# Kernel tuning notes

Measured on AMD Instinct MI355X. Metric: run time of the kernel, lower is better.

## Reference

```python
import jax, jax.numpy as jnp
import numpy as np

NUM_HEADS = 16
HEAD_DIM = 64  # embedding_dim 1024 / 16


def setup_inputs() -> dict:
    key = jax.random.key(0)
    k1, k2, k3, k4 = jax.random.split(key, 4)
    B, S, D = 2, 2048, 1024
    return {
        "query": jax.random.normal(k1, (B, S, D), dtype=jnp.float32),
        "key": jax.random.normal(k2, (B, S, D), dtype=jnp.float32),
        "value": jax.random.normal(k3, (B, S, D), dtype=jnp.float32),
        "W_out": jax.random.normal(k4, (D, D), dtype=jnp.float32) * (1.0 / np.sqrt(D)),
        "b_out": jnp.zeros((D,), dtype=jnp.float32),
    }


def reference(query, key, value, W_out, b_out):
    B, S, D = query.shape
    H, hd = NUM_HEADS, HEAD_DIM
    # NOTE: original forward never applies q_fc/k_fc/v_fc (transform ignores fc)
    q = query.reshape(B, S, H, hd).transpose(0, 2, 1, 3)  # [B,H,S,hd]
    k = key.reshape(B, S, H, hd).transpose(0, 2, 1, 3)
    v = value.reshape(B, S, H, hd).transpose(0, 2, 1, 3)
    scores = jnp.einsum("bhqd,bhkd->bhqk", q, k) / jnp.sqrt(jnp.float32(hd))
    probs = jax.nn.softmax(scores, axis=-1)  # mask=None, dropout=None
    ctx = jnp.einsum("bhqk,bhkd->bhqd", probs, v)
    ctx = ctx.transpose(0, 2, 1, 3).reshape(B, S, D)
    return ctx @ W_out.T + b_out
```

## Files before the change

### kernel.cpp

```cpp
#include <hip/hip_runtime.h>
#include <hip/hip_bf16.h>
#include <stdint.h>

#define NB 2
#define SEQ 2048
#define DIM 1024
#define NH 16
#define HD 64

typedef __attribute__((ext_vector_type(4))) float f32x4;
typedef __attribute__((ext_vector_type(16))) float f32x16;
typedef __attribute__((ext_vector_type(8))) short s16x8;
typedef __attribute__((ext_vector_type(4))) short s16x4;
typedef __attribute__((ext_vector_type(8))) __bf16 bf16x8;

static __device__ __forceinline__ short f2bf_rne(float x) {
  uint32_t u = __float_as_uint(x);
  u += 0x7fffu + ((u >> 16) & 1u);
  return (short)(u >> 16);
}
static __device__ __forceinline__ uint32_t pk_bf16(float a, float b) {
  __hip_bfloat162 h = __float22bfloat162_rn(float2{a, b});
  uint32_t u;
  __builtin_memcpy(&u, &h, 4);
  return u;
}
static __device__ __forceinline__ bf16x8 ldfrag(const short* p) {
  bf16x8 r;
  __builtin_memcpy(&r, p, 16);
  return r;
}
static __device__ __forceinline__ void glds16(const short* g, short* l) {
  __builtin_amdgcn_global_load_lds(
      (const __attribute__((address_space(1))) uint32_t*)g,
      (__attribute__((address_space(3))) uint32_t*)l, 16, 0, 0);
}

__global__ __launch_bounds__(256) void prep_all(const float* __restrict__ K,
                                                const float* __restrict__ V,
                                                const float* __restrict__ W,
                                                short* __restrict__ Kh,
                                                short* __restrict__ Vt,
                                                short* __restrict__ Wh) {
  __shared__ float vtile[64][65];
  const int tid = threadIdx.x;
  const int id = blockIdx.x;

  if (id >= 1024) {
    size_t idx = ((size_t)(id - 1024) * 256 + tid) * 8;
    f32x4 a = *(const f32x4*)(W + idx);
    f32x4 b = *(const f32x4*)(W + idx + 4);
    s16x8 o;
#pragma unroll
    for (int j = 0; j < 4; ++j) {
      o[j] = f2bf_rne(a[j]);
      o[4 + j] = f2bf_rne(b[j]);
    }
    *(s16x8*)(Wh + idx) = o;
    return;
  }

  const int t0 = (id & 31) * 64;
  const int bh = id >> 5;
  const int b = bh >> 4, h = bh & 15;

#pragma unroll
  for (int i = 0; i < 4; ++i) {
    int f = tid + 256 * i;
    int row = f >> 4;
    int col = (f & 15) * 4;
    const float* src = K + ((size_t)(b * SEQ + t0 + row)) * DIM + h * HD + col;
    f32x4 v = *(const f32x4*)src;
    s16x4 hi;
#pragma unroll
    for (int j = 0; j < 4; ++j) hi[j] = f2bf_rne(v[j]);
    *(s16x4*)(Kh + ((size_t)bh * SEQ + t0 + row) * HD + col) = hi;
  }
#pragma unroll
  for (int i = 0; i < 4; ++i) {
    int f = tid + 256 * i;
    int row = f >> 4;
    int col = (f & 15) * 4;
    const float* src = V + ((size_t)(b * SEQ + t0 + row)) * DIM + h * HD + col;
    f32x4 v = *(const f32x4*)src;
#pragma unroll
    for (int j = 0; j < 4; ++j) vtile[row][col + j] = v[j];
  }
  __syncthreads();
#pragma unroll
  for (int i = 0; i < 4; ++i) {
    int idx = tid + 256 * i;
    int d = idx >> 4;
    int kb = (idx & 15) * 4;
    int kp = (kb & ~12) | ((kb & 4) << 1) | ((kb & 8) >> 1);
    s16x4 o4;
#pragma unroll
    for (int j = 0; j < 4; ++j) o4[j] = f2bf_rne(vtile[kb + j][d]);
    *(s16x4*)(Vt + ((size_t)bh * HD + d) * SEQ + t0 + kp) = o4;
  }
}

#define QSCALE (0.125f * 1.44269504088896340736f)
#define NT_KV 32

static __device__ __forceinline__ f32x16 qk32(const short* kb, int kvh, int l32,
                                              int hl, const bf16x8* qh) {
  f32x16 s;
#pragma unroll
  for (int r = 0; r < 16; ++r) s[r] = 0.f;
#pragma unroll
  for (int ks = 0; ks < 4; ++ks) {
    bf16x8 kf =
        ldfrag(kb + (kvh * 32 + l32) * 64 + (((ks * 2 + hl) ^ (l32 & 7)) * 8));
    s = __builtin_amdgcn_mfma_f32_32x32x16_bf16(kf, qh[ks], s, 0, 0, 0);
  }
  return s;
}

static __device__ __forceinline__ void exppv32(const f32x16& sf, const short* vb,
                                               int kvh, int l32, int hl,
                                               f32x16* acc, float& den0,
                                               float& den1) {
#pragma unroll
  for (int tp = 0; tp < 2; ++tp) {
    uint32_t w[4];
#pragma unroll
    for (int j2 = 0; j2 < 4; ++j2) {
      float p0 = __builtin_amdgcn_exp2f(sf[tp * 8 + j2 * 2]);
      float p1 = __builtin_amdgcn_exp2f(sf[tp * 8 + j2 * 2 + 1]);
      den0 += p0;
      den1 += p1;
      w[j2] = pk_bf16(p0, p1);
    }
    bf16x8 pa;
    __builtin_memcpy(&pa, w, 16);
    const int ksg = kvh * 2 + tp;
#pragma unroll
    for (int dt = 0; dt < 2; ++dt) {
      bf16x8 vf = ldfrag(vb + (dt * 32 + l32) * 64 +
                         (((ksg * 2 + hl) ^ (l32 & 7)) * 8));
      acc[dt] =
          __builtin_amdgcn_mfma_f32_32x32x16_bf16(pa, vf, acc[dt], 0, 0, 0);
    }
  }
}

__global__ __launch_bounds__(512, 4) void attn(const float* __restrict__ Q,
                                               const short* __restrict__ Kh,
                                               const short* __restrict__ Vt,
                                               short* __restrict__ Ch) {
  __shared__ __align__(16) short kbuf[2][4096];
  __shared__ __align__(16) short vbuf[2][4096];
  __shared__ float dsh[8][64];

  const int tid = threadIdx.x;
  const int wv = tid >> 6, ln = tid & 63;
  const int l32 = ln & 31, hl = ln >> 5;
  const int qsub = wv >> 1, kvh = wv & 1;
  const int bh = blockIdx.y, b = bh >> 4, hh = bh & 15;
  const int q0 = blockIdx.x * 128 + qsub * 32;

  bf16x8 qh[4];
  {
    const float* qp = Q + ((size_t)(b * SEQ + q0 + l32)) * DIM + hh * HD + hl * 8;
#pragma unroll
    for (int ks = 0; ks < 4; ++ks) {
      short th[8];
#pragma unroll
      for (int j = 0; j < 8; ++j) th[j] = f2bf_rne(qp[ks * 16 + j] * QSCALE);
      __builtin_memcpy(&qh[ks], th, 16);
    }
  }

  f32x16 acc[2];
#pragma unroll
  for (int r = 0; r < 16; ++r) {
    acc[0][r] = 0.f;
    acc[1][r] = 0.f;
  }
  float den0 = 0.f, den1 = 0.f;

  const short* khg = Kh + (size_t)bh * SEQ * HD;
  const short* vtg = Vt + (size_t)bh * HD * SEQ;

  const int srow8 = ln >> 3;
  const int sg = ln & 7;
  const int sw = (sg ^ srow8) * 8;

#pragma unroll
  for (int i = 0; i < 3; ++i) {
    int c = wv * 3 + i;
    int lc = c & 7;
    int row = lc * 8 + srow8;
    if (c < 8)
      glds16(khg + (size_t)row * HD + sw, &kbuf[0][lc * 512]);
    else if (c < 16)
      glds16(vtg + (size_t)row * SEQ + sw, &vbuf[0][lc * 512]);
    else
      glds16(khg + (size_t)(64 + row) * HD + sw, &kbuf[1][lc * 512]);
  }
  __syncthreads();

  f32x16 sfA = qk32(&kbuf[0][0], kvh, l32, hl, qh);

  const int srow = wv * 8 + srow8;

  for (int t = 0; t < 30; t += 2) {
    __syncthreads();
    glds16(khg + (size_t)((t + 2) * 64 + srow) * HD + sw, &kbuf[0][wv * 512]);
    glds16(vtg + (size_t)srow * SEQ + (t + 1) * 64 + sw, &vbuf[1][wv * 512]);
    f32x16 sfB = qk32(&kbuf[1][0], kvh, l32, hl, qh);
    exppv32(sfA, &vbuf[0][0], kvh, l32, hl, acc, den0, den1);
    __syncthreads();
    glds16(khg + (size_t)((t + 3) * 64 + srow) * HD + sw, &kbuf[1][wv * 512]);
    glds16(vtg + (size_t)srow * SEQ + (t + 2) * 64 + sw, &vbuf[0][wv * 512]);
    sfA = qk32(&kbuf[0][0], kvh, l32, hl, qh);
    exppv32(sfB, &vbuf[1][0], kvh, l32, hl, acc, den0, den1);
  }
  __syncthreads();
  glds16(vtg + (size_t)srow * SEQ + 31 * 64 + sw, &vbuf[1][wv * 512]);
  f32x16 sfT = qk32(&kbuf[1][0], kvh, l32, hl, qh);
  exppv32(sfA, &vbuf[0][0], kvh, l32, hl, acc, den0, den1);
  __syncthreads();
  exppv32(sfT, &vbuf[1][0], kvh, l32, hl, acc, den0, den1);

  float den = den0 + den1;
  den += __shfl_xor(den, 32);

  f32x16 give, keep;
  if (kvh == 0) {
    give = acc[1];
    keep = acc[0];
  } else {
    give = acc[0];
    keep = acc[1];
  }

  __syncthreads();
  float* xr = (wv < 4) ? (float*)&kbuf[0][0] : (float*)&vbuf[0][0];
  *(f32x16*)(xr + (wv & 3) * 1024 + ln * 16) = give;
  dsh[wv][ln] = den;
  __syncthreads();

  float dtot = den + dsh[wv ^ 1][ln];
  float invd = 1.0f / dtot;
  float inv_r[16];
#pragma unroll
  for (int r = 0; r < 16; ++r)
    inv_r[r] = __shfl(invd, (r & 3) + 8 * (r >> 2) + 4 * hl, 64);

  f32x16 oth = *(const f32x16*)(xr + ((wv ^ 1) & 3) * 1024 + ln * 16);
#pragma unroll
  for (int r = 0; r < 16; ++r) {
    float cs = keep[r] + oth[r];
    int row = (r & 3) + 8 * (r >> 2) + 4 * hl;
    size_t off =
        ((size_t)(b * SEQ + q0 + row)) * DIM + hh * HD + kvh * 32 + l32;
    Ch[off] = f2bf_rne(cs * inv_r[r]);
  }
}

__global__ __launch_bounds__(256, 4) void proj(const short* __restrict__ Ah,
                                               const short* __restrict__ Wh,
                                               const float* __restrict__ bias,
                                               float* __restrict__ OUT) {
  __shared__ __align__(16) short ash[2][4096];
  __shared__ __align__(16) short wsh[2][4096];
  const int tid = threadIdx.x;
  const int wv = tid >> 6, ln = tid & 63;
  const int l32 = ln & 31, hl = ln >> 5;
  const int wm = wv & 1, wn = wv >> 1;
  const int m0 = blockIdx.x * 64, n0 = blockIdx.y * 64;

  f32x16 acc;
#pragma unroll
  for (int r = 0; r < 16; ++r) acc[r] = 0.f;

  const int srow8 = ln >> 3, sg = ln & 7;
  const int sw = (sg ^ srow8) * 8;

#pragma unroll
  for (int i = 0; i < 4; ++i) {
    int c = wv * 4 + i;
    int row = (c & 7) * 8 + srow8;
    if (c < 8)
      glds16(Ah + (size_t)(m0 + row) * DIM + sw, ash[0] + (c & 7) * 512);
    else
      glds16(Wh + (size_t)(n0 + row) * DIM + sw, wsh[0] + (c & 7) * 512);
  }

  for (int kt = 0; kt < DIM / 64; ++kt) {
    __syncthreads();
    if (kt + 1 < DIM / 64) {
      const int kk = (kt + 1) * 64;
      const int bn = (kt + 1) & 1;
#pragma unroll
      for (int i = 0; i < 4; ++i) {
        int c = wv * 4 + i;
        int row = (c & 7) * 8 + srow8;
        if (c < 8)
          glds16(Ah + (size_t)(m0 + row) * DIM + kk + sw, ash[bn] + (c & 7) * 512);
        else
          glds16(Wh + (size_t)(n0 + row) * DIM + kk + sw, wsh[bn] + (c & 7) * 512);
      }
    }
    const short* ab = ash[kt & 1];
    const short* wb = wsh[kt & 1];
#pragma unroll
    for (int ks = 0; ks < 4; ++ks) {
      bf16x8 af = ldfrag(ab + (wm * 32 + l32) * 64 + (((ks * 2 + hl) ^ (l32 & 7)) * 8));
      bf16x8 wf = ldfrag(wb + (wn * 32 + l32) * 64 + (((ks * 2 + hl) ^ (l32 & 7)) * 8));
      acc = __builtin_amdgcn_mfma_f32_32x32x16_bf16(af, wf, acc, 0, 0, 0);
    }
  }

  float bs = bias[n0 + wn * 32 + l32];
#pragma unroll
  for (int r = 0; r < 16; ++r) {
    int row = m0 + wm * 32 + (r & 3) + 8 * (r >> 2) + 4 * hl;
    int col = n0 + wn * 32 + l32;
    OUT[(size_t)row * DIM + col] = acc[r] + bs;
  }
}

extern "C" void kernel_launch(void* const* d_in, const int* in_sizes, int n_in,
                              void* d_out, int out_size, void* d_ws, size_t ws_size,
                              hipStream_t stream) {
  const float* Q = (const float*)d_in[0];
  const float* K = (const float*)d_in[1];
  const float* V = (const float*)d_in[2];
  const float* W = (const float*)d_in[3];
  const float* bias = (const float*)d_in[4];
  float* OUT = (float*)d_out;

  char* ws = (char*)d_ws;
  short* Kh = (short*)(ws + ((size_t)0 << 20));
  short* Vt = (short*)(ws + ((size_t)8 << 20));
  short* Ch = (short*)(ws + ((size_t)16 << 20));
  short* Wh = (short*)(ws + ((size_t)24 << 20));

  prep_all<<<dim3(1536), 256, 0, stream>>>(K, V, W, Kh, Vt, Wh);
  attn<<<dim3(SEQ / 128, NB * NH), 512, 0, stream>>>(Q, Kh, Vt, Ch);
  proj<<<dim3((NB * SEQ) / 64, DIM / 64), 256, 0, stream>>>(Ch, Wh, bias, OUT);
}
```

Measured before the change: 161.6 us.

## Halve attention block to 64 queries with 256 threads and raise wave priority around MFMA

The attention kernel now uses 4 waves per block covering 64 queries instead of 8 waves covering 128, so it launches twice as many blocks. Each wave issues twice as many K/V tile loads into LDS. s_setprio is raised around the QK/PV compute sections so compute waves are favoured over waves issuing loads. The change aims for better CU load balance and more scheduling flexibility, at the cost of twice the total K/V traffic from memory into LDS and less reuse per loaded tile.

```diff
diff --git a/kernel.cpp b/kernel.cpp
--- a/kernel.cpp
+++ b/kernel.cpp
@@ -145,20 +145,20 @@
   }
 }
 
-__global__ __launch_bounds__(512, 4) void attn(const float* __restrict__ Q,
+__global__ __launch_bounds__(256, 4) void attn(const float* __restrict__ Q,
                                                const short* __restrict__ Kh,
                                                const short* __restrict__ Vt,
                                                short* __restrict__ Ch) {
   __shared__ __align__(16) short kbuf[2][4096];
   __shared__ __align__(16) short vbuf[2][4096];
-  __shared__ float dsh[8][64];
+  __shared__ float dsh[4][64];
 
   const int tid = threadIdx.x;
   const int wv = tid >> 6, ln = tid & 63;
   const int l32 = ln & 31, hl = ln >> 5;
   const int qsub = wv >> 1, kvh = wv & 1;
   const int bh = blockIdx.y, b = bh >> 4, hh = bh & 15;
-  const int q0 = blockIdx.x * 128 + qsub * 32;
+  const int q0 = blockIdx.x * 64 + qsub * 32;
 
   bf16x8 qh[4];
   {
@@ -188,8 +188,8 @@
   const int sw = (sg ^ srow8) * 8;
 
 #pragma unroll
-  for (int i = 0; i < 3; ++i) {
-    int c = wv * 3 + i;
+  for (int i = 0; i < 6; ++i) {
+    int c = wv * 6 + i;
     int lc = c & 7;
     int row = lc * 8 + srow8;
     if (c < 8)
@@ -203,24 +203,43 @@
 
   f32x16 sfA = qk32(&kbuf[0][0], kvh, l32, hl, qh);
 
-  const int srow = wv * 8 + srow8;
-
   for (int t = 0; t < 30; t += 2) {
     __syncthreads();
-    glds16(khg + (size_t)((t + 2) * 64 + srow) * HD + sw, &kbuf[0][wv * 512]);
-    glds16(vtg + (size_t)srow * SEQ + (t + 1) * 64 + sw, &vbuf[1][wv * 512]);
+#pragma unroll
+    for (int i = 0; i < 2; ++i) {
+      int lc = wv * 2 + i;
+      int row = lc * 8 + srow8;
+      glds16(khg + (size_t)((t + 2) * 64 + row) * HD + sw, &kbuf[0][lc * 512]);
+      glds16(vtg + (size_t)row * SEQ + (t + 1) * 64 + sw, &vbuf[1][lc * 512]);
+    }
+    __builtin_amdgcn_s_setprio(1);
     f32x16 sfB = qk32(&kbuf[1][0], kvh, l32, hl, qh);
     exppv32(sfA, &vbuf[0][0], kvh, l32, hl, acc, den0, den1);
+    __builtin_amdgcn_s_setprio(0);
     __syncthreads();
-    glds16(khg + (size_t)((t + 3) * 64 + srow) * HD + sw, &kbuf[1][wv * 512]);
-    glds16(vtg + (size_t)srow * SEQ + (t + 2) * 64 + sw, &vbuf[0][wv * 512]);
+#pragma unroll
+    for (int i = 0; i < 2; ++i) {
+      int lc = wv * 2 + i;
+      int row = lc * 8 + srow8;
+      glds16(khg + (size_t)((t + 3) * 64 + row) * HD + sw, &kbuf[1][lc * 512]);
+      glds16(vtg + (size_t)row * SEQ + (t + 2) * 64 + sw, &vbuf[0][lc * 512]);
+    }
+    __builtin_amdgcn_s_setprio(1);
     sfA = qk32(&kbuf[0][0], kvh, l32, hl, qh);
     exppv32(sfB, &vbuf[1][0], kvh, l32, hl, acc, den0, den1);
-  }
-  __syncthreads();
-  glds16(vtg + (size_t)srow * SEQ + 31 * 64 + sw, &vbuf[1][wv * 512]);
+    __builtin_amdgcn_s_setprio(0);
+  }
+  __syncthreads();
+#pragma unroll
+  for (int i = 0; i < 2; ++i) {
+    int lc = wv * 2 + i;
+    int row = lc * 8 + srow8;
+    glds16(vtg + (size_t)row * SEQ + 31 * 64 + sw, &vbuf[1][lc * 512]);
+  }
+  __builtin_amdgcn_s_setprio(1);
   f32x16 sfT = qk32(&kbuf[1][0], kvh, l32, hl, qh);
   exppv32(sfA, &vbuf[0][0], kvh, l32, hl, acc, den0, den1);
+  __builtin_amdgcn_s_setprio(0);
   __syncthreads();
   exppv32(sfT, &vbuf[1][0], kvh, l32, hl, acc, den0, den1);
 
@@ -237,8 +256,8 @@
   }
 
   __syncthreads();
-  float* xr = (wv < 4) ? (float*)&kbuf[0][0] : (float*)&vbuf[0][0];
-  *(f32x16*)(xr + (wv & 3) * 1024 + ln * 16) = give;
+  float* xr = (wv < 2) ? (float*)&kbuf[0][0] : (float*)&vbuf[0][0];
+  *(f32x16*)(xr + (wv & 1) * 1024 + ln * 16) = give;
   dsh[wv][ln] = den;
   __syncthreads();
 
@@ -249,7 +268,7 @@
   for (int r = 0; r < 16; ++r)
     inv_r[r] = __shfl(invd, (r & 3) + 8 * (r >> 2) + 4 * hl, 64);
 
-  f32x16 oth = *(const f32x16*)(xr + ((wv ^ 1) & 3) * 1024 + ln * 16);
+  f32x16 oth = *(const f32x16*)(xr + ((wv ^ 1) & 1) * 1024 + ln * 16);
 #pragma unroll
   for (int r = 0; r < 16; ++r) {
     float cs = keep[r] + oth[r];
@@ -340,6 +359,6 @@
   short* Wh = (short*)(ws + ((size_t)24 << 20));
 
   prep_all<<<dim3(1536), 256, 0, stream>>>(K, V, W, Kh, Vt, Wh);
-  attn<<<dim3(SEQ / 128, NB * NH), 512, 0, stream>>>(Q, Kh, Vt, Ch);
+  attn<<<dim3(SEQ / 64, NB * NH), 256, 0, stream>>>(Q, Kh, Vt, Ch);
   proj<<<dim3((NB * SEQ) / 64, DIM / 64), 256, 0, stream>>>(Ch, Wh, bias, OUT);
 }
```

New measurement: 207.4 us. 1.28x slower.

## Load K fragments directly from global into registers instead of LDS

Applied to the files above, without the earlier changes.

K tiles are no longer staged through shared memory. Each lane now loads its own K fragments from global memory straight into registers, and the QK MFMA is moved after the PV step so the loads have time to complete. This removes the K shared-memory traffic and reduces LDS footprint, but gives up cross-wave sharing of K loads, so every wave fetches K from global/L2 on its own, and it raises register pressure.

```diff
diff --git a/kernel.cpp b/kernel.cpp
--- a/kernel.cpp
+++ b/kernel.cpp
@@ -103,20 +103,6 @@
 #define QSCALE (0.125f * 1.44269504088896340736f)
 #define NT_KV 32
 
-static __device__ __forceinline__ f32x16 qk32(const short* kb, int kvh, int l32,
-                                              int hl, const bf16x8* qh) {
-  f32x16 s;
-#pragma unroll
-  for (int r = 0; r < 16; ++r) s[r] = 0.f;
-#pragma unroll
-  for (int ks = 0; ks < 4; ++ks) {
-    bf16x8 kf =
-        ldfrag(kb + (kvh * 32 + l32) * 64 + (((ks * 2 + hl) ^ (l32 & 7)) * 8));
-    s = __builtin_amdgcn_mfma_f32_32x32x16_bf16(kf, qh[ks], s, 0, 0, 0);
-  }
-  return s;
-}
-
 static __device__ __forceinline__ void exppv32(const f32x16& sf, const short* vb,
                                                int kvh, int l32, int hl,
                                                f32x16* acc, float& den0,
@@ -145,12 +131,23 @@
   }
 }
 
+static __device__ __forceinline__ f32x16 qkreg(const bf16x8* kf,
+                                               const bf16x8* qh) {
+  f32x16 s;
+#pragma unroll
+  for (int r = 0; r < 16; ++r) s[r] = 0.f;
+#pragma unroll
+  for (int ks = 0; ks < 4; ++ks)
+    s = __builtin_amdgcn_mfma_f32_32x32x16_bf16(kf[ks], qh[ks], s, 0, 0, 0);
+  return s;
+}
+
 __global__ __launch_bounds__(512, 4) void attn(const float* __restrict__ Q,
                                                const short* __restrict__ Kh,
                                                const short* __restrict__ Vt,
                                                short* __restrict__ Ch) {
-  __shared__ __align__(16) short kbuf[2][4096];
   __shared__ __align__(16) short vbuf[2][4096];
+  __shared__ __align__(16) float xbuf[4096];
   __shared__ float dsh[8][64];
 
   const int tid = threadIdx.x;
@@ -180,47 +177,46 @@
   }
   float den0 = 0.f, den1 = 0.f;
 
-  const short* khg = Kh + (size_t)bh * SEQ * HD;
+  const short* khg =
+      Kh + (size_t)bh * SEQ * HD + (size_t)(kvh * 32 + l32) * HD + hl * 8;
   const short* vtg = Vt + (size_t)bh * HD * SEQ;
 
   const int srow8 = ln >> 3;
   const int sg = ln & 7;
   const int sw = (sg ^ srow8) * 8;
-
-#pragma unroll
-  for (int i = 0; i < 3; ++i) {
-    int c = wv * 3 + i;
-    int lc = c & 7;
-    int row = lc * 8 + srow8;
-    if (c < 8)
-      glds16(khg + (size_t)row * HD + sw, &kbuf[0][lc * 512]);
-    else if (c < 16)
-      glds16(vtg + (size_t)row * SEQ + sw, &vbuf[0][lc * 512]);
-    else
-      glds16(khg + (size_t)(64 + row) * HD + sw, &kbuf[1][lc * 512]);
-  }
-  __syncthreads();
-
-  f32x16 sfA = qk32(&kbuf[0][0], kvh, l32, hl, qh);
-
   const int srow = wv * 8 + srow8;
+
+  bf16x8 kf0[4];
+#pragma unroll
+  for (int ks = 0; ks < 4; ++ks) kf0[ks] = ldfrag(khg + ks * 16);
+  glds16(vtg + (size_t)srow * SEQ + sw, &vbuf[0][wv * 512]);
+  f32x16 sfA = qkreg(kf0, qh);
 
   for (int t = 0; t < 30; t += 2) {
     __syncthreads();
-    glds16(khg + (size_t)((t + 2) * 64 + srow) * HD + sw, &kbuf[0][wv * 512]);
+    bf16x8 kfa[4];
+#pragma unroll
+    for (int ks = 0; ks < 4; ++ks)
+      kfa[ks] = ldfrag(khg + (t + 1) * 4096 + ks * 16);
     glds16(vtg + (size_t)srow * SEQ + (t + 1) * 64 + sw, &vbuf[1][wv * 512]);
-    f32x16 sfB = qk32(&kbuf[1][0], kvh, l32, hl, qh);
     exppv32(sfA, &vbuf[0][0], kvh, l32, hl, acc, den0, den1);
+    f32x16 sfB = qkreg(kfa, qh);
     __syncthreads();
-    glds16(khg + (size_t)((t + 3) * 64 + srow) * HD + sw, &kbuf[1][wv * 512]);
+    bf16x8 kfb[4];
+#pragma unroll
+    for (int ks = 0; ks < 4; ++ks)
+      kfb[ks] = ldfrag(khg + (t + 2) * 4096 + ks * 16);
     glds16(vtg + (size_t)srow * SEQ + (t + 2) * 64 + sw, &vbuf[0][wv * 512]);
-    sfA = qk32(&kbuf[0][0], kvh, l32, hl, qh);
     exppv32(sfB, &vbuf[1][0], kvh, l32, hl, acc, den0, den1);
-  }
-  __syncthreads();
+    sfA = qkreg(kfb, qh);
+  }
+  __syncthreads();
+  bf16x8 kfl[4];
+#pragma unroll
+  for (int ks = 0; ks < 4; ++ks) kfl[ks] = ldfrag(khg + 31 * 4096 + ks * 16);
   glds16(vtg + (size_t)srow * SEQ + 31 * 64 + sw, &vbuf[1][wv * 512]);
-  f32x16 sfT = qk32(&kbuf[1][0], kvh, l32, hl, qh);
   exppv32(sfA, &vbuf[0][0], kvh, l32, hl, acc, den0, den1);
+  f32x16 sfT = qkreg(kfl, qh);
   __syncthreads();
   exppv32(sfT, &vbuf[1][0], kvh, l32, hl, acc, den0, den1);
 
@@ -237,7 +233,7 @@
   }
 
   __syncthreads();
-  float* xr = (wv < 4) ? (float*)&kbuf[0][0] : (float*)&vbuf[0][0];
+  float* xr = (wv < 4) ? &xbuf[0] : (float*)&vbuf[0][0];
   *(f32x16*)(xr + (wv & 3) * 1024 + ln * 16) = give;
   dsh[wv][ln] = den;
   __syncthreads();
```

After: 182.5 us. 1.13x slower.
